# Kernel tuning notes

Hardware: AMD Instinct MI355X
Metric: run time of the kernel (lower is better)

Reference implementation:

```python
import jax, jax.numpy as jnp
import numpy as np

STRIDE = 8
OUT = 96                 # feature map size fh = fw
SEARCH = OUT * STRIDE    # 768, search image size
RATIOS = [0.33, 0.5, 1.0, 2.0, 3.0]
SCALES = [4, 8, 16]
PRE_NMS = 1024
POST_NMS = 256
NMS_THRESH = 0.7


def _make_anchors():
    # anchor widths/heights per (ratio, scale), base size = stride * scale
    ws, hs = [], []
    for r in RATIOS:
        for s in SCALES:
            ws.append(STRIDE * s / np.sqrt(r))
            hs.append(STRIDE * s * np.sqrt(r))
    ws = np.asarray(ws, np.float32)  # [A]
    hs = np.asarray(hs, np.float32)
    ori = SEARCH // 2 - (OUT // 2) * STRIDE
    c = ori + STRIDE * np.arange(OUT, dtype=np.float32)
    cy, cx = np.meshgrid(c, c, indexing="ij")  # [OUT, OUT]
    x1 = cx[None] - ws[:, None, None] * 0.5  # [A, OUT, OUT]
    y1 = cy[None] - hs[:, None, None] * 0.5
    x2 = cx[None] + ws[:, None, None] * 0.5
    y2 = cy[None] + hs[:, None, None] * 0.5
    return np.stack([x1, y1, x2, y2], axis=-1).reshape(-1, 4)  # [A*K, 4]


def setup_inputs() -> dict:
    key = jax.random.key(0)
    k1, k2 = jax.random.split(key)
    pred_cls = jax.random.normal(k1, (32, 30, 96, 96), jnp.float32)
    pred_reg = jax.random.normal(k2, (32, 60, 96, 96), jnp.float32) * 0.2
    anchors = jnp.asarray(_make_anchors())
    return {"pred_cls": pred_cls, "pred_reg": pred_reg, "anchors": anchors}


def _nms_pad(boxes, scores):
    """boxes [N,4] sorted by score desc, scores [N]. Returns [POST_NMS,5] padded."""
    x1, y1, x2, y2 = boxes[:, 0], boxes[:, 1], boxes[:, 2], boxes[:, 3]
    areas = (x2 - x1 + 1.0) * (y2 - y1 + 1.0)
    ix1 = jnp.maximum(x1[:, None], x1[None, :])
    iy1 = jnp.maximum(y1[:, None], y1[None, :])
    ix2 = jnp.minimum(x2[:, None], x2[None, :])
    iy2 = jnp.minimum(y2[:, None], y2[None, :])
    inter = jnp.maximum(ix2 - ix1 + 1.0, 0.0) * jnp.maximum(iy2 - iy1 + 1.0, 0.0)
    iou = inter / (areas[:, None] + areas[None, :] - inter)
    n = boxes.shape[0]
    idxs = jnp.arange(n)

    def body(keep, i):
        sup = keep[i] & (iou[i] > NMS_THRESH) & (idxs > i)
        return keep & ~sup, None

    keep, _ = jax.lax.scan(body, jnp.ones((n,), bool), idxs)
    pos = jnp.cumsum(keep) - 1
    dst = jnp.where(keep & (pos < POST_NMS), pos, POST_NMS)  # pad row for dropped
    rows = jnp.concatenate([scores[:, None], boxes], axis=1)  # [N,5] score first
    out = jnp.zeros((POST_NMS + 1, 5), boxes.dtype).at[dst].set(rows)
    return out[:POST_NMS]


def reference(pred_cls, pred_reg, anchors):
    b, a2, h, w = pred_cls.shape
    A = a2 // 2
    # log-softmax over the 2-way fg/bg channel; take foreground log-probs
    logp = jax.nn.log_softmax(pred_cls.reshape(b, 2, A, h, w), axis=1)
    scores = logp[:, 1].reshape(b, -1)  # [b, A*h*w]
    # deltas: (b,4A,h,w) -> (b,4,A,h,w) -> (b,A,h,w,4) -> (b,A*h*w,4)
    deltas = pred_reg.reshape(b, 4, A, h, w).transpose(0, 2, 3, 4, 1).reshape(b, -1, 4)
    aw = anchors[:, 2] - anchors[:, 0] + 1.0
    ah = anchors[:, 3] - anchors[:, 1] + 1.0
    acx = anchors[:, 0] + 0.5 * aw
    acy = anchors[:, 1] + 0.5 * ah
    dx, dy, dw, dh = deltas[..., 0], deltas[..., 1], deltas[..., 2], deltas[..., 3]
    pcx = dx * aw + acx
    pcy = dy * ah + acy
    pw = jnp.exp(dw) * aw
    ph = jnp.exp(dh) * ah
    boxes = jnp.stack([pcx - 0.5 * pw, pcy - 0.5 * ph, pcx + 0.5 * pw, pcy + 0.5 * ph], axis=-1)
    boxes = jnp.clip(boxes, 0.0, SEARCH - 1.0)  # clip to image
    top_s, top_i = jax.lax.top_k(scores, PRE_NMS)  # per-image pre-NMS top-k
    top_b = jnp.take_along_axis(boxes, top_i[..., None], axis=1)  # [b,PRE,4]
    return jax.vmap(_nms_pad)(top_b, top_s)  # [b, POST_NMS, 5]
```

## Files before the change

kernel.cpp:

```cpp
#include <hip/hip_runtime.h>
#include <stdint.h>

#define NANCH 138240
#define NANCH4 34560
#define B_CNT 32
#define PRE 1024
#define POST 256
#define BINS 8192
#define CAP 4096
#define SBLK 9
#define V4PB 3840
#define CNT_STRIDE 64
#define PAD_KEY 0xFFFFFFFFFFFFFFFFull

typedef unsigned long long u64;
typedef unsigned short u16;

__device__ __forceinline__ unsigned key32(float sc) {
    unsigned u = __float_as_uint(sc);
    unsigned s = (u & 0x80000000u) ? ~u : (u | 0x80000000u);
    return ~s;
}

__device__ __forceinline__ unsigned key_of(float x0, float x1) {
    float m  = fmaxf(x0, x1);
    float e0 = expf(x0 - m);
    float e1 = expf(x1 - m);
    float sc = (x1 - m) - logf(e0 + e1);
    return key32(sc);
}

__device__ __forceinline__ void decode_box(const float* __restrict__ reg,
                                           const float* __restrict__ anch,
                                           int b, int idx, float box[4]) {
    const float* rb = reg + (size_t)b * 4 * NANCH;
    float dx = rb[idx];
    float dy = rb[idx + NANCH];
    float dw = rb[idx + 2 * NANCH];
    float dh = rb[idx + 3 * NANCH];
    float ax1 = anch[idx * 4 + 0], ay1 = anch[idx * 4 + 1];
    float ax2 = anch[idx * 4 + 2], ay2 = anch[idx * 4 + 3];
    float aw  = __fadd_rn(__fsub_rn(ax2, ax1), 1.0f);
    float ah  = __fadd_rn(__fsub_rn(ay2, ay1), 1.0f);
    float acx = __fadd_rn(ax1, __fmul_rn(0.5f, aw));
    float acy = __fadd_rn(ay1, __fmul_rn(0.5f, ah));
    float pcx = __fadd_rn(__fmul_rn(dx, aw), acx);
    float pcy = __fadd_rn(__fmul_rn(dy, ah), acy);
    float pw  = __fmul_rn(expf(dw), aw);
    float ph  = __fmul_rn(expf(dh), ah);
    float hx  = __fmul_rn(0.5f, pw);
    float hy  = __fmul_rn(0.5f, ph);
    box[0] = fminf(fmaxf(__fsub_rn(pcx, hx), 0.0f), 767.0f);
    box[1] = fminf(fmaxf(__fsub_rn(pcy, hy), 0.0f), 767.0f);
    box[2] = fminf(fmaxf(__fadd_rn(pcx, hx), 0.0f), 767.0f);
    box[3] = fminf(fmaxf(__fadd_rn(pcy, hy), 0.0f), 767.0f);
}

__global__ __launch_bounds__(1024) void score_kernel(const float* __restrict__ cls,
                                                     u16* __restrict__ part,
                                                     int* __restrict__ cnt) {
    __shared__ unsigned h[BINS];
    const int b = blockIdx.y;
    const int t = threadIdx.x;
    if (blockIdx.x == 0 && t == 0) cnt[b * CNT_STRIDE] = 0;
    for (int i = t; i < BINS; i += 1024) h[i] = 0;
    __syncthreads();
    const float4* cb4 = (const float4*)(cls + (size_t)b * 2 * NANCH);
    const int base4 = blockIdx.x * V4PB;
    for (int k = 0; k < 4; ++k) {
        int off = k * 1024 + t;
        if (off < V4PB) {
            int g4 = base4 + off;
            float4 a0 = cb4[g4];
            float4 a1 = cb4[g4 + NANCH4];
            atomicAdd(&h[key32(a1.x - a0.x) >> 19], 1u);
            atomicAdd(&h[key32(a1.y - a0.y) >> 19], 1u);
            atomicAdd(&h[key32(a1.z - a0.z) >> 19], 1u);
            atomicAdd(&h[key32(a1.w - a0.w) >> 19], 1u);
        }
    }
    __syncthreads();
    u16* pb = part + ((size_t)(b * SBLK + blockIdx.x)) * BINS;
    for (int i = t; i < BINS; i += 1024) pb[i] = (u16)h[i];
}

__global__ __launch_bounds__(1024) void compact_kernel(const float* __restrict__ cls,
                                                       const u16* __restrict__ part,
                                                       int* __restrict__ cnt,
                                                       u64* __restrict__ cand) {
    __shared__ u64 loc[CAP];
    __shared__ unsigned s_part[1024];
    __shared__ int s_b;
    __shared__ int lcnt;
    __shared__ int gbase;
    const int b = blockIdx.y;
    const int t = threadIdx.x;
    if (t == 0) lcnt = 0;

    unsigned bin[8];
    #pragma unroll
    for (int i = 0; i < 8; ++i) bin[i] = 0;
    const u16* pb = part + (size_t)b * SBLK * BINS;
    for (int s = 0; s < SBLK; ++s) {
        const u16* ps = pb + (size_t)s * BINS + t * 8;
        #pragma unroll
        for (int i = 0; i < 8; ++i) bin[i] += ps[i];
    }
    unsigned seg = 0;
    #pragma unroll
    for (int i = 0; i < 8; ++i) seg += bin[i];
    s_part[t] = seg;
    __syncthreads();
    for (int off = 1; off < 1024; off <<= 1) {
        unsigned v = (t >= off) ? s_part[t - off] : 0u;
        __syncthreads();
        s_part[t] += v;
        __syncthreads();
    }
    unsigned incl = s_part[t];
    unsigned excl = incl - seg;
    if (incl >= PRE && excl < PRE) {
        unsigned cum = excl;
        int bs = t * 8 + 7;
        for (int i = 0; i < 8; ++i) {
            if (cum + bin[i] >= PRE) { bs = t * 8 + i; break; }
            cum += bin[i];
        }
        s_b = bs;
    }
    __syncthreads();
    const int bs = s_b + 1;

    const float4* cb4 = (const float4*)(cls + (size_t)b * 2 * NANCH);
    const int base4 = blockIdx.x * V4PB;
    for (int k = 0; k < 4; ++k) {
        int off = k * 1024 + t;
        if (off < V4PB) {
            int g4 = base4 + off;
            float4 a0 = cb4[g4];
            float4 a1 = cb4[g4 + NANCH4];
            float x0[4] = {a0.x, a0.y, a0.z, a0.w};
            float x1[4] = {a1.x, a1.y, a1.z, a1.w};
            #pragma unroll
            for (int j = 0; j < 4; ++j) {
                unsigned dk = key32(x1[j] - x0[j]);
                if ((int)(dk >> 19) <= bs) {
                    unsigned key = key_of(x0[j], x1[j]);
                    int pos = atomicAdd(&lcnt, 1);
                    if (pos < CAP)
                        loc[pos] = ((u64)key << 32) | (unsigned)(g4 * 4 + j);
                }
            }
        }
    }
    __syncthreads();
    int n = lcnt; if (n > CAP) n = CAP;
    if (t == 0) gbase = atomicAdd(&cnt[b * CNT_STRIDE], n);
    __syncthreads();
    const int gb = gbase;
    for (int i = t; i < n; i += 1024) {
        int g = gb + i;
        if (g < CAP) cand[(size_t)b * CAP + g] = loc[i];
    }
}

__global__ __launch_bounds__(512) void lsort_kernel(const int* __restrict__ cnt,
                                                    u64* __restrict__ cand) {
    __shared__ u64 s[1024];
    const int c = blockIdx.x;
    const int b = blockIdx.y;
    const int t = threadIdx.x;
    int n = cnt[b * CNT_STRIDE]; if (n > CAP) n = CAP;
    u64* seg = cand + (size_t)b * CAP + c * 1024;
    const int base = c * 1024;
    for (int i = t; i < 1024; i += 512)
        s[i] = (base + i < n) ? seg[i] : PAD_KEY;
    __syncthreads();
    for (int k = 2; k <= 1024; k <<= 1) {
        for (int j = k >> 1; j > 0; j >>= 1) {
            int i  = ((t & ~(j - 1)) << 1) | (t & (j - 1));
            int p  = i | j;
            bool up = ((i & k) == 0);
            u64 a = s[i], bb = s[p];
            if ((a > bb) == up) { s[i] = bb; s[p] = a; }
            __syncthreads();
        }
    }
    for (int i = t; i < 1024; i += 512) seg[i] = s[i];
}

__global__ __launch_bounds__(1024) void merge_kernel(const u64* __restrict__ cand,
                                                     const float* __restrict__ reg,
                                                     const float* __restrict__ anch,
                                                     float* __restrict__ topS,
                                                     float* __restrict__ topB) {
    __shared__ u64 runs[CAP];
    __shared__ u64 outk[PRE];
    const int b = blockIdx.x;
    const int t = threadIdx.x;
    for (int i = t; i < CAP; i += 1024) runs[i] = cand[(size_t)b * CAP + i];
    __syncthreads();

    #pragma unroll
    for (int r = 0; r < 4; ++r) {
        u64 x = runs[r * 1024 + t];
        int rank = t;
        #pragma unroll
        for (int q = 0; q < 4; ++q) {
            if (q == r) continue;
            const u64* run = &runs[q * 1024];
            int lo = 0, hi = 1024;
            while (lo < hi) {
                int mid = (lo + hi) >> 1;
                if (run[mid] < x) lo = mid + 1; else hi = mid;
            }
            rank += lo;
        }
        if (rank < PRE) outk[rank] = x;
    }
    __syncthreads();

    u64 key = outk[t];
    int idx = (int)(key & 0xFFFFFFFFu);
    unsigned ks = (unsigned)(key >> 32);
    unsigned s  = ~ks;
    unsigned u  = (s & 0x80000000u) ? (s & 0x7FFFFFFFu) : ~s;
    float sc = __uint_as_float(u);
    float box[4];
    decode_box(reg, anch, b, idx, box);
    topS[b * PRE + t] = sc;
    float* tb = topB + ((size_t)b * PRE + t) * 4;
    tb[0] = box[0]; tb[1] = box[1]; tb[2] = box[2]; tb[3] = box[3];
}

__global__ __launch_bounds__(1024) void mask_kernel(const float* __restrict__ topB,
                                                    u64* __restrict__ masks) {
    const int w = blockIdx.x;
    const int b = blockIdx.y;
    const int i = threadIdx.x;
    __shared__ float sx1[64], sy1[64], sx2[64], sy2[64], sar[64];
    if (i < 64) {
        const float* p = topB + ((size_t)b * PRE + w * 64 + i) * 4;
        float x1 = p[0], y1 = p[1], x2 = p[2], y2 = p[3];
        sx1[i] = x1; sy1[i] = y1; sx2[i] = x2; sy2[i] = y2;
        sar[i] = __fmul_rn(__fadd_rn(__fsub_rn(x2, x1), 1.0f),
                           __fadd_rn(__fsub_rn(y2, y1), 1.0f));
    }
    __syncthreads();
    const int jbase = w * 64;
    u64* dst = &masks[((size_t)b * PRE + i) * 16 + w];
    if (i >= jbase + 63) { *dst = 0ull; return; }
    const float* p = topB + ((size_t)b * PRE + i) * 4;
    float x1 = p[0], y1 = p[1], x2 = p[2], y2 = p[3];
    float ar = __fmul_rn(__fadd_rn(__fsub_rn(x2, x1), 1.0f),
                         __fadd_rn(__fsub_rn(y2, y1), 1.0f));
    u64 m = 0ull;
    for (int j = 0; j < 64; j++) {
        int jj = jbase + j;
        if (jj > i) {
            float ix1 = fmaxf(x1, sx1[j]);
            float iy1 = fmaxf(y1, sy1[j]);
            float ix2 = fminf(x2, sx2[j]);
            float iy2 = fminf(y2, sy2[j]);
            float iw = fmaxf(__fadd_rn(__fsub_rn(ix2, ix1), 1.0f), 0.0f);
            float ih = fmaxf(__fadd_rn(__fsub_rn(iy2, iy1), 1.0f), 0.0f);
            float inter = __fmul_rn(iw, ih);
            float denom = __fsub_rn(__fadd_rn(ar, sar[j]), inter);
            float iou = __fdiv_rn(inter, denom);
            if (iou > 0.7f) m |= (1ull << j);
        }
    }
    *dst = m;
}

__device__ __forceinline__ u64 shfl_xor_u64(u64 v, int lanemask) {
    int lo = __shfl_xor((int)(v & 0xFFFFFFFFull), lanemask);
    int hi = __shfl_xor((int)(v >> 32), lanemask);
    return ((u64)(unsigned)hi << 32) | (unsigned)lo;
}

__global__ __launch_bounds__(64) void nms_kernel(const u64* __restrict__ masks,
                                                 const float* __restrict__ topS,
                                                 const float* __restrict__ topB,
                                                 float* __restrict__ out) {
    const int b = blockIdx.x;
    const int t = threadIdx.x;
    __shared__ u64 rem[16];
    __shared__ int kept[POST];
    __shared__ int s_nk;
    if (t < 16) rem[t] = 0ull;
    __syncthreads();

    const u64* mb = masks + (size_t)b * PRE * 16;
    const int w = t >> 2, g = t & 3;
    int prefix = 0;

    u64 dv_cur = mb[(size_t)t * 16 + 0];
    u64 cw_cur[16];
    #pragma unroll
    for (int k = 0; k < 16; ++k)
        cw_cur[k] = mb[((size_t)(g * 16 + k)) * 16 + w];

    for (int c = 0; c < 16; ++c) {
        u64 dv_nxt = 0ull;
        u64 cw_nxt[16];
        if (c < 15) {
            const u64* nb = mb + (size_t)(c + 1) * 64 * 16;
            dv_nxt = nb[(size_t)t * 16 + (c + 1)];
            #pragma unroll
            for (int k = 0; k < 16; ++k)
                cw_nxt[k] = nb[((size_t)(g * 16 + k)) * 16 + w];
        } else {
            #pragma unroll
            for (int k = 0; k < 16; ++k) cw_nxt[k] = 0ull;
        }

        u64 alive = ~rem[c];
        int dlo = (int)(dv_cur & 0xFFFFFFFFull);
        int dhi = (int)(dv_cur >> 32);

        for (int l = 0; l < 64; ++l) {
            unsigned lo = (unsigned)__builtin_amdgcn_readlane(dlo, l);
            unsigned hi = (unsigned)__builtin_amdgcn_readlane(dhi, l);
            u64 dl = ((u64)hi << 32) | lo;
            u64 a = (alive >> l) & 1ull;
            alive &= ~(a ? dl : 0ull);
        }

        if ((alive >> t) & 1ull) {
            int pos = prefix + (int)__popcll(alive & ((1ull << t) - 1ull));
            if (pos < POST) kept[pos] = c * 64 + t;
        }
        prefix += (int)__popcll(alive);

        u64 acc = 0ull;
        #pragma unroll
        for (int k = 0; k < 16; ++k)
            if ((alive >> (g * 16 + k)) & 1ull) acc |= cw_cur[k];
        acc |= shfl_xor_u64(acc, 1);
        acc |= shfl_xor_u64(acc, 2);
        __syncthreads();
        if (g == 0 && w > c) rem[w] |= acc;
        __syncthreads();

        if (prefix >= POST) break;

        dv_cur = dv_nxt;
        #pragma unroll
        for (int k = 0; k < 16; ++k) cw_cur[k] = cw_nxt[k];
    }

    if (t == 0) s_nk = (prefix < POST) ? prefix : POST;
    __syncthreads();
    const int n = s_nk;

    float* ob = out + (size_t)b * POST * 5;
    for (int r = t; r < POST; r += 64) {
        if (r < n) {
            int i = kept[r];
            ob[r * 5 + 0] = topS[b * PRE + i];
            const float* tb = topB + ((size_t)b * PRE + i) * 4;
            ob[r * 5 + 1] = tb[0];
            ob[r * 5 + 2] = tb[1];
            ob[r * 5 + 3] = tb[2];
            ob[r * 5 + 4] = tb[3];
        } else {
            ob[r * 5 + 0] = 0.0f; ob[r * 5 + 1] = 0.0f; ob[r * 5 + 2] = 0.0f;
            ob[r * 5 + 3] = 0.0f; ob[r * 5 + 4] = 0.0f;
        }
    }
}

extern "C" void kernel_launch(void* const* d_in, const int* in_sizes, int n_in,
                              void* d_out, int out_size, void* d_ws, size_t ws_size,
                              hipStream_t stream) {
    const float* cls  = (const float*)d_in[0];
    const float* reg  = (const float*)d_in[1];
    const float* anch = (const float*)d_in[2];

    char* ws = (char*)d_ws;
    int*   cnt   = (int*)ws;
    float* topS  = (float*)(ws + 8448);
    float* topB  = (float*)(ws + 139520);
    u64*   cand  = (u64*)(ws + 663808);
    u16*   part  = (u16*)(ws + 1712384);
    u64*   masks = (u64*)(ws + 1712384);

    score_kernel  <<<dim3(SBLK, B_CNT), 1024, 0, stream>>>(cls, part, cnt);
    compact_kernel<<<dim3(SBLK, B_CNT), 1024, 0, stream>>>(cls, part, cnt, cand);
    lsort_kernel  <<<dim3(4, B_CNT), 512, 0, stream>>>(cnt, cand);
    merge_kernel  <<<B_CNT, 1024, 0, stream>>>(cand, reg, anch, topS, topB);
    mask_kernel   <<<dim3(16, B_CNT), 1024, 0, stream>>>(topB, masks);
    nms_kernel    <<<B_CNT, 64, 0, stream>>>(masks, topS, topB, (float*)d_out);
}
```

Before: 104.2 us.

## Cache 16-bit score keys for compaction and fuse local sort into merge

The score pass now also writes the top 16 bits of each logit-difference key to a workspace array. The compact pass then filters on these 2-byte keys and only gathers the full cls logits for the few survivors, instead of re-reading 8 bytes per anchor. The separate 4x1024 bitonic local-sort kernel is removed and its work moves into the merge kernel, which saves one launch but sorts the four runs inside only 32 blocks. This adds a 256KB-per-batch extra write and scattered reads for candidates, and may lower parallelism in the sort stage.

```diff
diff --git a/kernel.cpp b/kernel.cpp
--- a/kernel.cpp
+++ b/kernel.cpp
@@ -10,6 +10,7 @@
 #define CAP 4096
 #define SBLK 9
 #define V4PB 3840
+#define U8PB 1920
 #define CNT_STRIDE 64
 #define PAD_KEY 0xFFFFFFFFFFFFFFFFull
 
@@ -57,6 +58,7 @@
 }
 
 __global__ __launch_bounds__(1024) void score_kernel(const float* __restrict__ cls,
+                                                     u16* __restrict__ dk16,
                                                      u16* __restrict__ part,
                                                      int* __restrict__ cnt) {
     __shared__ unsigned h[BINS];
@@ -66,6 +68,7 @@
     for (int i = t; i < BINS; i += 1024) h[i] = 0;
     __syncthreads();
     const float4* cb4 = (const float4*)(cls + (size_t)b * 2 * NANCH);
+    ushort4* db4 = (ushort4*)(dk16 + (size_t)b * NANCH);
     const int base4 = blockIdx.x * V4PB;
     for (int k = 0; k < 4; ++k) {
         int off = k * 1024 + t;
@@ -73,10 +76,16 @@
             int g4 = base4 + off;
             float4 a0 = cb4[g4];
             float4 a1 = cb4[g4 + NANCH4];
-            atomicAdd(&h[key32(a1.x - a0.x) >> 19], 1u);
-            atomicAdd(&h[key32(a1.y - a0.y) >> 19], 1u);
-            atomicAdd(&h[key32(a1.z - a0.z) >> 19], 1u);
-            atomicAdd(&h[key32(a1.w - a0.w) >> 19], 1u);
+            unsigned k0 = key32(a1.x - a0.x);
+            unsigned k1 = key32(a1.y - a0.y);
+            unsigned k2 = key32(a1.z - a0.z);
+            unsigned k3 = key32(a1.w - a0.w);
+            db4[g4] = make_ushort4((u16)(k0 >> 16), (u16)(k1 >> 16),
+                                   (u16)(k2 >> 16), (u16)(k3 >> 16));
+            atomicAdd(&h[k0 >> 19], 1u);
+            atomicAdd(&h[k1 >> 19], 1u);
+            atomicAdd(&h[k2 >> 19], 1u);
+            atomicAdd(&h[k3 >> 19], 1u);
         }
     }
     __syncthreads();
@@ -85,6 +94,7 @@
 }
 
 __global__ __launch_bounds__(1024) void compact_kernel(const float* __restrict__ cls,
+                                                       const u16* __restrict__ dk16,
                                                        const u16* __restrict__ part,
                                                        int* __restrict__ cnt,
                                                        u64* __restrict__ cand) {
@@ -131,24 +141,26 @@
     __syncthreads();
     const int bs = s_b + 1;
 
-    const float4* cb4 = (const float4*)(cls + (size_t)b * 2 * NANCH);
-    const int base4 = blockIdx.x * V4PB;
-    for (int k = 0; k < 4; ++k) {
+    const float* cb = cls + (size_t)b * 2 * NANCH;
+    const uint4* db4 = (const uint4*)(dk16 + (size_t)b * NANCH);
+    const int base8 = blockIdx.x * U8PB;
+    for (int k = 0; k < 2; ++k) {
         int off = k * 1024 + t;
-        if (off < V4PB) {
-            int g4 = base4 + off;
-            float4 a0 = cb4[g4];
-            float4 a1 = cb4[g4 + NANCH4];
-            float x0[4] = {a0.x, a0.y, a0.z, a0.w};
-            float x1[4] = {a1.x, a1.y, a1.z, a1.w};
+        if (off < U8PB) {
+            int g8 = base8 + off;
+            uint4 v = db4[g8];
+            unsigned w[4] = {v.x, v.y, v.z, v.w};
             #pragma unroll
-            for (int j = 0; j < 4; ++j) {
-                unsigned dk = key32(x1[j] - x0[j]);
-                if ((int)(dk >> 19) <= bs) {
-                    unsigned key = key_of(x0[j], x1[j]);
+            for (int i = 0; i < 8; ++i) {
+                unsigned dk = (w[i >> 1] >> ((i & 1) * 16)) & 0xFFFFu;
+                if ((int)(dk >> 3) <= bs) {
+                    int idx = g8 * 8 + i;
+                    float x0 = cb[idx];
+                    float x1 = cb[idx + NANCH];
+                    unsigned key = key_of(x0, x1);
                     int pos = atomicAdd(&lcnt, 1);
                     if (pos < CAP)
-                        loc[pos] = ((u64)key << 32) | (unsigned)(g4 * 4 + j);
+                        loc[pos] = ((u64)key << 32) | (unsigned)idx;
                 }
             }
         }
@@ -164,42 +176,35 @@
     }
 }
 
-__global__ __launch_bounds__(512) void lsort_kernel(const int* __restrict__ cnt,
-                                                    u64* __restrict__ cand) {
-    __shared__ u64 s[1024];
-    const int c = blockIdx.x;
-    const int b = blockIdx.y;
-    const int t = threadIdx.x;
-    int n = cnt[b * CNT_STRIDE]; if (n > CAP) n = CAP;
-    u64* seg = cand + (size_t)b * CAP + c * 1024;
-    const int base = c * 1024;
-    for (int i = t; i < 1024; i += 512)
-        s[i] = (base + i < n) ? seg[i] : PAD_KEY;
-    __syncthreads();
-    for (int k = 2; k <= 1024; k <<= 1) {
-        for (int j = k >> 1; j > 0; j >>= 1) {
-            int i  = ((t & ~(j - 1)) << 1) | (t & (j - 1));
-            int p  = i | j;
-            bool up = ((i & k) == 0);
-            u64 a = s[i], bb = s[p];
-            if ((a > bb) == up) { s[i] = bb; s[p] = a; }
-            __syncthreads();
-        }
-    }
-    for (int i = t; i < 1024; i += 512) seg[i] = s[i];
-}
-
-__global__ __launch_bounds__(1024) void merge_kernel(const u64* __restrict__ cand,
-                                                     const float* __restrict__ reg,
-                                                     const float* __restrict__ anch,
-                                                     float* __restrict__ topS,
-                                                     float* __restrict__ topB) {
+__global__ __launch_bounds__(1024) void sortmerge_kernel(const u64* __restrict__ cand,
+                                                         const int* __restrict__ cnt,
+                                                         const float* __restrict__ reg,
+                                                         const float* __restrict__ anch,
+                                                         float* __restrict__ topS,
+                                                         float* __restrict__ topB) {
     __shared__ u64 runs[CAP];
     __shared__ u64 outk[PRE];
     const int b = blockIdx.x;
     const int t = threadIdx.x;
-    for (int i = t; i < CAP; i += 1024) runs[i] = cand[(size_t)b * CAP + i];
-    __syncthreads();
+    int n = cnt[b * CNT_STRIDE]; if (n > CAP) n = CAP;
+    for (int i = t; i < CAP; i += 1024)
+        runs[i] = (i < n) ? cand[(size_t)b * CAP + i] : PAD_KEY;
+    __syncthreads();
+
+    for (int k = 2; k <= 1024; k <<= 1) {
+        for (int j = k >> 1; j > 0; j >>= 1) {
+            #pragma unroll
+            for (int pp = 0; pp < 2; ++pp) {
+                int p = t + pp * 1024;
+                int i = ((p & ~(j - 1)) << 1) | (p & (j - 1));
+                int q = i | j;
+                bool up = (((i & 1023) & k) == 0);
+                u64 a = runs[i], c = runs[q];
+                if ((a > c) == up) { runs[i] = c; runs[q] = a; }
+            }
+            __syncthreads();
+        }
+    }
 
     #pragma unroll
     for (int r = 0; r < 4; ++r) {
@@ -385,11 +390,11 @@
     u64*   cand  = (u64*)(ws + 663808);
     u16*   part  = (u16*)(ws + 1712384);
     u64*   masks = (u64*)(ws + 1712384);
-
-    score_kernel  <<<dim3(SBLK, B_CNT), 1024, 0, stream>>>(cls, part, cnt);
-    compact_kernel<<<dim3(SBLK, B_CNT), 1024, 0, stream>>>(cls, part, cnt, cand);
-    lsort_kernel  <<<dim3(4, B_CNT), 512, 0, stream>>>(cnt, cand);
-    merge_kernel  <<<B_CNT, 1024, 0, stream>>>(cand, reg, anch, topS, topB);
-    mask_kernel   <<<dim3(16, B_CNT), 1024, 0, stream>>>(topB, masks);
-    nms_kernel    <<<B_CNT, 64, 0, stream>>>(masks, topS, topB, (float*)d_out);
-}
+    u16*   dk16  = (u16*)(ws + 6430976);
+
+    score_kernel    <<<dim3(SBLK, B_CNT), 1024, 0, stream>>>(cls, dk16, part, cnt);
+    compact_kernel  <<<dim3(SBLK, B_CNT), 1024, 0, stream>>>(cls, dk16, part, cnt, cand);
+    sortmerge_kernel<<<B_CNT, 1024, 0, stream>>>(cand, cnt, reg, anch, topS, topB);
+    mask_kernel     <<<dim3(16, B_CNT), 1024, 0, stream>>>(topB, masks);
+    nms_kernel      <<<B_CNT, 64, 0, stream>>>(masks, topS, topB, (float*)d_out);
+}
```

Result: slower. 119.0 us (+14.2%).
